# Kernel optimization log

Measured on AMD Instinct MI355X. Metric: run time of the kernel, lower is better.

Reference implementation:

```python
import jax, jax.numpy as jnp
import numpy as np

N_NODES = 100000
N_EDGES = 6400000
D_FEAT = 5
OUT_CLASSES = 16


def setup_inputs() -> dict:
    key = jax.random.key(0)
    k1, k2, k3, k4, k5 = jax.random.split(key, 5)
    h = jax.random.normal(k1, (N_NODES, D_FEAT), dtype=jnp.float32)
    src = jax.random.randint(k2, (N_EDGES,), 0, N_NODES, dtype=jnp.int64)
    dst = jax.random.randint(k3, (N_EDGES,), 0, N_NODES, dtype=jnp.int64)
    W_weight = jax.random.normal(k4, (OUT_CLASSES, 2 * D_FEAT), dtype=jnp.float32) * 0.1
    W_bias = jax.random.normal(k5, (OUT_CLASSES,), dtype=jnp.float32) * 0.1
    return {"h": h, "src": src, "dst": dst, "W_weight": W_weight, "W_bias": W_bias}


def reference(h, src, dst, W_weight, W_bias):
    # Edge-wise: gather src/dst node features, concat -> [E, 2D], linear -> [E, C]
    h_u = h[src]                      # [E, D]
    h_v = h[dst]                      # [E, D]
    feat = jnp.concatenate([h_u, h_v], axis=1)  # [E, 2D]
    score = feat @ W_weight.T + W_bias           # [E, C]
    return score
```

## Files before the change

kernel.cpp:

```cpp
#include <hip/hip_runtime.h>


typedef float f4v __attribute__((ext_vector_type(4)));

constexpr int C = 16;
constexpr int TWO_D = 10;
constexpr int D = 5;
constexpr int N_NODES = 100000;

template <int CTRL>
__device__ __forceinline__ float qperm(float x) {
    return __int_as_float(
        __builtin_amdgcn_mov_dpp(__float_as_int(x), CTRL, 0xF, 0xF, true));
}

__global__ __launch_bounds__(256) void pad_h_kernel(
    const float* __restrict__ h, float* __restrict__ h8, int total8)
{
    for (int i = blockIdx.x * blockDim.x + threadIdx.x; i < total8;
         i += gridDim.x * blockDim.x) {
        const int row = i >> 3, k = i & 7;
        h8[i] = (k < D) ? h[row * D + k] : 0.0f;
    }
}

__global__ __launch_bounds__(256) void edge_mlp_v2(
    const float* __restrict__ h8,
    const int* __restrict__ src,
    const int* __restrict__ dst,
    const float* __restrict__ Ww,
    const float* __restrict__ Wb,
    float* __restrict__ out,
    int totalItems)
{
    __shared__ float sW[C * TWO_D + C];
    for (int i = threadIdx.x; i < C * TWO_D + C; i += blockDim.x)
        sW[i] = (i < C * TWO_D) ? Ww[i] : Wb[i - C * TWO_D];
    __syncthreads();

    const int tid0 = blockIdx.x * blockDim.x + threadIdx.x;
    const int q = tid0 & 3;
    const bool hiHalf = (q & 1) != 0;
    const bool isV = (q >= 2);

    float w[4][TWO_D], bias[4];
#pragma unroll
    for (int j = 0; j < 4; ++j) {
        const int c = q * 4 + j;
#pragma unroll
        for (int k = 0; k < TWO_D; ++k) w[j][k] = sW[c * TWO_D + k];
        bias[j] = sW[C * TWO_D + c];
    }

    const int stride = gridDim.x * blockDim.x;
    const int stride2 = stride * 2;
    const int TImax = totalItems - 1;

    auto clampE = [&](int g) { return (g < TImax ? g : TImax) >> 2; };

    auto body = [&](const f4v gv, int gout, bool doStore) {
        f4v o1;
        o1[0] = qperm<0xB1>(gv[0]); o1[1] = qperm<0xB1>(gv[1]);
        o1[2] = qperm<0xB1>(gv[2]); o1[3] = qperm<0xB1>(gv[3]);
        const f4v mlo = hiHalf ? o1 : gv;
        const float m4 = hiHalf ? gv[0] : o1[0];
        f4v olo;
        olo[0] = qperm<0x4E>(mlo[0]); olo[1] = qperm<0x4E>(mlo[1]);
        olo[2] = qperm<0x4E>(mlo[2]); olo[3] = qperm<0x4E>(mlo[3]);
        const float o4 = qperm<0x4E>(m4);

        const float u0 = isV ? olo[0] : mlo[0];
        const float u1 = isV ? olo[1] : mlo[1];
        const float u2 = isV ? olo[2] : mlo[2];
        const float u3 = isV ? olo[3] : mlo[3];
        const float u4 = isV ? o4     : m4;
        const float v0 = isV ? mlo[0] : olo[0];
        const float v1 = isV ? mlo[1] : olo[1];
        const float v2 = isV ? mlo[2] : olo[2];
        const float v3 = isV ? mlo[3] : olo[3];
        const float v4 = isV ? m4     : o4;

        f4v r;
#pragma unroll
        for (int j = 0; j < 4; ++j) {
            float a = bias[j];
            a += u0 * w[j][0] + u1 * w[j][1] + u2 * w[j][2] + u3 * w[j][3] + u4 * w[j][4];
            a += v0 * w[j][5] + v1 * w[j][6] + v2 * w[j][7] + v3 * w[j][8] + v4 * w[j][9];
            r[j] = a;
        }
        if (doStore)
            __builtin_nontemporal_store(r, reinterpret_cast<f4v*>(out + (size_t)gout * 4));
    };

    int g = tid0;
    int eA = clampE(g), eB = clampE(g + stride);
    int sA = __builtin_nontemporal_load(src + eA);
    int dA = __builtin_nontemporal_load(dst + eA);
    int sB = __builtin_nontemporal_load(src + eB);
    int dB = __builtin_nontemporal_load(dst + eB);

    for (; g < totalItems; g += stride2) {
        const int rA = isV ? dA : sA;
        const int rB = isV ? dB : sB;
        const f4v gvA = *reinterpret_cast<const f4v*>(h8 + (size_t)rA * 8 + (hiHalf ? 4 : 0));
        const f4v gvB = *reinterpret_cast<const f4v*>(h8 + (size_t)rB * 8 + (hiHalf ? 4 : 0));

        const int gn = g + stride2;
        eA = clampE(gn); eB = clampE(gn + stride);
        sA = __builtin_nontemporal_load(src + eA);
        dA = __builtin_nontemporal_load(dst + eA);
        sB = __builtin_nontemporal_load(src + eB);
        dB = __builtin_nontemporal_load(dst + eB);

        body(gvA, g, true);
        body(gvB, g + stride, (g + stride) < totalItems);
    }
}

__global__ __launch_bounds__(256) void edge_mlp_v1(
    const float* __restrict__ h,
    const int* __restrict__ src,
    const int* __restrict__ dst,
    const float* __restrict__ Ww,
    const float* __restrict__ Wb,
    float* __restrict__ out,
    int totalItems)
{
    __shared__ float sW[C * TWO_D + C];
    for (int i = threadIdx.x; i < C * TWO_D + C; i += blockDim.x)
        sW[i] = (i < C * TWO_D) ? Ww[i] : Wb[i - C * TWO_D];
    __syncthreads();

    const int tid0 = blockIdx.x * blockDim.x + threadIdx.x;
    const int q = tid0 & 3;
    float w[4][TWO_D], bias[4];
#pragma unroll
    for (int j = 0; j < 4; ++j) {
        const int c = q * 4 + j;
#pragma unroll
        for (int k = 0; k < TWO_D; ++k) w[j][k] = sW[c * TWO_D + k];
        bias[j] = sW[C * TWO_D + c];
    }

    const int stride = gridDim.x * blockDim.x;
    for (int g = tid0; g < totalItems; g += stride) {
        const int e = g >> 2;
        const int s = src[e];
        const int d = dst[e];
        const float* pu = h + s * 5;
        const float* pv = h + d * 5;
        const float u0 = pu[0], u1 = pu[1], u2 = pu[2], u3 = pu[3], u4 = pu[4];
        const float v0 = pv[0], v1 = pv[1], v2 = pv[2], v3 = pv[3], v4 = pv[4];
        float4 r;
        float* rp = &r.x;
#pragma unroll
        for (int j = 0; j < 4; ++j) {
            float a = bias[j];
            a += u0 * w[j][0] + u1 * w[j][1] + u2 * w[j][2] + u3 * w[j][3] + u4 * w[j][4];
            a += v0 * w[j][5] + v1 * w[j][6] + v2 * w[j][7] + v3 * w[j][8] + v4 * w[j][9];
            rp[j] = a;
        }
        *reinterpret_cast<float4*>(out + (size_t)g * 4) = r;
    }
}

extern "C" void kernel_launch(void* const* d_in, const int* in_sizes, int n_in,
                              void* d_out, int out_size, void* d_ws, size_t ws_size,
                              hipStream_t stream) {
    const float* h   = (const float*)d_in[0];
    const int*   src = (const int*)d_in[1];
    const int*   dst = (const int*)d_in[2];
    const float* Ww  = (const float*)d_in[3];
    const float* Wb  = (const float*)d_in[4];
    float* out = (float*)d_out;

    const int E = in_sizes[1];
    const int totalItems = E * 4;

    const size_t needWs = (size_t)N_NODES * 8 * sizeof(float);
    if (d_ws != nullptr && ws_size >= needWs) {
        float* h8 = (float*)d_ws;
        pad_h_kernel<<<1024, 256, 0, stream>>>(h, h8, N_NODES * 8);
        edge_mlp_v2<<<4096, 256, 0, stream>>>(h8, src, dst, Ww, Wb, out, totalItems);
    } else {
        edge_mlp_v1<<<4096, 256, 0, stream>>>(h, src, dst, Ww, Wb, out, totalItems);
    }
}
```

Before: 549.2 us.

## Drop padded h copy, load overlapping unaligned rows, deepen gather prefetch

Removes the pad_h pre-kernel and its workspace copy. Each lane of a quad now does an unaligned 4-float load straight from the 5-wide h rows, at offset 0 or 1, and rebuilds the 5 features with DPP lane shuffles. The main loop also prefetches the gathered h rows one iteration ahead, on top of the index prefetch, to hide gather latency. The trade is unaligned loads that may straddle cache lines, and extra registers held for the in-flight rows.

```diff
diff --git a/kernel.cpp b/kernel.cpp
--- a/kernel.cpp
+++ b/kernel.cpp
@@ -2,11 +2,10 @@
 
 
 typedef float f4v __attribute__((ext_vector_type(4)));
+typedef f4v uf4v __attribute__((aligned(4)));
 
 constexpr int C = 16;
 constexpr int TWO_D = 10;
-constexpr int D = 5;
-constexpr int N_NODES = 100000;
 
 template <int CTRL>
 __device__ __forceinline__ float qperm(float x) {
@@ -14,18 +13,8 @@
         __builtin_amdgcn_mov_dpp(__float_as_int(x), CTRL, 0xF, 0xF, true));
 }
 
-__global__ __launch_bounds__(256) void pad_h_kernel(
-    const float* __restrict__ h, float* __restrict__ h8, int total8)
-{
-    for (int i = blockIdx.x * blockDim.x + threadIdx.x; i < total8;
-         i += gridDim.x * blockDim.x) {
-        const int row = i >> 3, k = i & 7;
-        h8[i] = (k < D) ? h[row * D + k] : 0.0f;
-    }
-}
-
-__global__ __launch_bounds__(256) void edge_mlp_v2(
-    const float* __restrict__ h8,
+__global__ __launch_bounds__(256) void edge_mlp_v3(
+    const float* __restrict__ h,
     const int* __restrict__ src,
     const int* __restrict__ dst,
     const float* __restrict__ Ww,
@@ -40,7 +29,7 @@
 
     const int tid0 = blockIdx.x * blockDim.x + threadIdx.x;
     const int q = tid0 & 3;
-    const bool hiHalf = (q & 1) != 0;
+    const bool odd = (q & 1) != 0;
     const bool isV = (q >= 2);
 
     float w[4][TWO_D], bias[4];
@@ -58,27 +47,31 @@
 
     auto clampE = [&](int g) { return (g < TImax ? g : TImax) >> 2; };
 
-    auto body = [&](const f4v gv, int gout, bool doStore) {
-        f4v o1;
-        o1[0] = qperm<0xB1>(gv[0]); o1[1] = qperm<0xB1>(gv[1]);
-        o1[2] = qperm<0xB1>(gv[2]); o1[3] = qperm<0xB1>(gv[3]);
-        const f4v mlo = hiHalf ? o1 : gv;
-        const float m4 = hiHalf ? gv[0] : o1[0];
-        f4v olo;
-        olo[0] = qperm<0x4E>(mlo[0]); olo[1] = qperm<0x4E>(mlo[1]);
-        olo[2] = qperm<0x4E>(mlo[2]); olo[3] = qperm<0x4E>(mlo[3]);
-        const float o4 = qperm<0x4E>(m4);
+    auto loadrow = [&](int s, int d) -> f4v {
+        const int r = isV ? d : s;
+        const float* p = h + (size_t)r * 5 + (odd ? 1 : 0);
+        return *reinterpret_cast<const uf4v*>(p);
+    };
 
-        const float u0 = isV ? olo[0] : mlo[0];
-        const float u1 = isV ? olo[1] : mlo[1];
-        const float u2 = isV ? olo[2] : mlo[2];
-        const float u3 = isV ? olo[3] : mlo[3];
-        const float u4 = isV ? o4     : m4;
-        const float v0 = isV ? mlo[0] : olo[0];
-        const float v1 = isV ? mlo[1] : olo[1];
-        const float v2 = isV ? mlo[2] : olo[2];
-        const float v3 = isV ? mlo[3] : olo[3];
-        const float v4 = isV ? m4     : o4;
+    auto body = [&](const f4v m, int gout, bool doStore) {
+        const float o0 = qperm<0xB1>(m[0]);
+        const float o3 = qperm<0xB1>(m[3]);
+        const float a0 = odd ? o0   : m[0];
+        const float a1 = odd ? m[0] : m[1];
+        const float a2 = odd ? m[1] : m[2];
+        const float a3 = odd ? m[2] : m[3];
+        const float a4 = odd ? m[3] : o3;
+        const float b0 = qperm<0x4E>(a0);
+        const float b1 = qperm<0x4E>(a1);
+        const float b2 = qperm<0x4E>(a2);
+        const float b3 = qperm<0x4E>(a3);
+        const float b4 = qperm<0x4E>(a4);
+
+        const float u0 = isV ? b0 : a0, v0 = isV ? a0 : b0;
+        const float u1 = isV ? b1 : a1, v1 = isV ? a1 : b1;
+        const float u2 = isV ? b2 : a2, v2 = isV ? a2 : b2;
+        const float u3 = isV ? b3 : a3, v3 = isV ? a3 : b3;
+        const float u4 = isV ? b4 : a4, v4 = isV ? a4 : b4;
 
         f4v r;
 #pragma unroll
@@ -92,75 +85,34 @@
             __builtin_nontemporal_store(r, reinterpret_cast<f4v*>(out + (size_t)gout * 4));
     };
 
-    int g = tid0;
-    int eA = clampE(g), eB = clampE(g + stride);
+    int eA = clampE(tid0), eB = clampE(tid0 + stride);
     int sA = __builtin_nontemporal_load(src + eA);
     int dA = __builtin_nontemporal_load(dst + eA);
     int sB = __builtin_nontemporal_load(src + eB);
     int dB = __builtin_nontemporal_load(dst + eB);
-
-    for (; g < totalItems; g += stride2) {
-        const int rA = isV ? dA : sA;
-        const int rB = isV ? dB : sB;
-        const f4v gvA = *reinterpret_cast<const f4v*>(h8 + (size_t)rA * 8 + (hiHalf ? 4 : 0));
-        const f4v gvB = *reinterpret_cast<const f4v*>(h8 + (size_t)rB * 8 + (hiHalf ? 4 : 0));
-
-        const int gn = g + stride2;
+    f4v gA = loadrow(sA, dA);
+    f4v gB = loadrow(sB, dB);
+    {
+        const int gn = tid0 + stride2;
         eA = clampE(gn); eB = clampE(gn + stride);
         sA = __builtin_nontemporal_load(src + eA);
         dA = __builtin_nontemporal_load(dst + eA);
         sB = __builtin_nontemporal_load(src + eB);
         dB = __builtin_nontemporal_load(dst + eB);
-
-        body(gvA, g, true);
-        body(gvB, g + stride, (g + stride) < totalItems);
-    }
-}
-
-__global__ __launch_bounds__(256) void edge_mlp_v1(
-    const float* __restrict__ h,
-    const int* __restrict__ src,
-    const int* __restrict__ dst,
-    const float* __restrict__ Ww,
-    const float* __restrict__ Wb,
-    float* __restrict__ out,
-    int totalItems)
-{
-    __shared__ float sW[C * TWO_D + C];
-    for (int i = threadIdx.x; i < C * TWO_D + C; i += blockDim.x)
-        sW[i] = (i < C * TWO_D) ? Ww[i] : Wb[i - C * TWO_D];
-    __syncthreads();
-
-    const int tid0 = blockIdx.x * blockDim.x + threadIdx.x;
-    const int q = tid0 & 3;
-    float w[4][TWO_D], bias[4];
-#pragma unroll
-    for (int j = 0; j < 4; ++j) {
-        const int c = q * 4 + j;
-#pragma unroll
-        for (int k = 0; k < TWO_D; ++k) w[j][k] = sW[c * TWO_D + k];
-        bias[j] = sW[C * TWO_D + c];
     }
 
-    const int stride = gridDim.x * blockDim.x;
-    for (int g = tid0; g < totalItems; g += stride) {
-        const int e = g >> 2;
-        const int s = src[e];
-        const int d = dst[e];
-        const float* pu = h + s * 5;
-        const float* pv = h + d * 5;
-        const float u0 = pu[0], u1 = pu[1], u2 = pu[2], u3 = pu[3], u4 = pu[4];
-        const float v0 = pv[0], v1 = pv[1], v2 = pv[2], v3 = pv[3], v4 = pv[4];
-        float4 r;
-        float* rp = &r.x;
-#pragma unroll
-        for (int j = 0; j < 4; ++j) {
-            float a = bias[j];
-            a += u0 * w[j][0] + u1 * w[j][1] + u2 * w[j][2] + u3 * w[j][3] + u4 * w[j][4];
-            a += v0 * w[j][5] + v1 * w[j][6] + v2 * w[j][7] + v3 * w[j][8] + v4 * w[j][9];
-            rp[j] = a;
-        }
-        *reinterpret_cast<float4*>(out + (size_t)g * 4) = r;
+    for (int g = tid0; g < totalItems; g += stride2) {
+        const f4v nA = loadrow(sA, dA);
+        const f4v nB = loadrow(sB, dB);
+        const int gn = g + 2 * stride2;
+        eA = clampE(gn); eB = clampE(gn + stride);
+        sA = __builtin_nontemporal_load(src + eA);
+        dA = __builtin_nontemporal_load(dst + eA);
+        sB = __builtin_nontemporal_load(src + eB);
+        dB = __builtin_nontemporal_load(dst + eB);
+        body(gA, g, true);
+        body(gB, g + stride, (g + stride) < totalItems);
+        gA = nA; gB = nB;
     }
 }
 
@@ -177,12 +129,5 @@
     const int E = in_sizes[1];
     const int totalItems = E * 4;
 
-    const size_t needWs = (size_t)N_NODES * 8 * sizeof(float);
-    if (d_ws != nullptr && ws_size >= needWs) {
-        float* h8 = (float*)d_ws;
-        pad_h_kernel<<<1024, 256, 0, stream>>>(h, h8, N_NODES * 8);
-        edge_mlp_v2<<<4096, 256, 0, stream>>>(h8, src, dst, Ww, Wb, out, totalItems);
-    } else {
-        edge_mlp_v1<<<4096, 256, 0, stream>>>(h, src, dst, Ww, Wb, out, totalItems);
-    }
+    edge_mlp_v3<<<4096, 256, 0, stream>>>(h, src, dst, Ww, Wb, out, totalItems);
 }
```

Result: no change. 555.2 us (+1.1%).
